# Optimization experiments

Measured on AMD Instinct MI355X. Metric: run time of the kernel, lower is better.

The kernel has to match this reference:

```python
import jax, jax.numpy as jnp
import numpy as np

# dims matching init_kwargs
D_MODEL = 2048
D_STATE = 64
D_CONV = 4
EXPAND = 2
HEADDIM = 128
NGROUPS = 1
CHUNK = 256
D_INNER = EXPAND * D_MODEL          # 4096
NHEADS = D_INNER // HEADDIM          # 32
CONV_DIM = D_INNER + 2 * NGROUPS * D_STATE      # 4224
D_IN_PROJ = 2 * D_INNER + 2 * NGROUPS * D_STATE + NHEADS  # 8352
BATCH = 2
SEQ = 4096  # multiple of CHUNK -> pad_to_block_length is a no-op
LN_EPS = 1e-5


def setup_inputs() -> dict:
    key = jax.random.key(0)
    ks = jax.random.split(key, 8)
    u = jax.random.normal(ks[0], (BATCH, SEQ, D_MODEL), jnp.float32)
    in_proj_w = jax.random.normal(ks[1], (D_IN_PROJ, D_MODEL), jnp.float32) * 0.02
    in_proj_b = jnp.zeros((D_IN_PROJ,), jnp.float32)
    conv_w = jax.random.normal(ks[2], (CONV_DIM, 1, D_CONV), jnp.float32) * 0.2
    conv_b = jnp.zeros((CONV_DIM,), jnp.float32)
    # dt_bias init as in the module (inverse-softplus of dt in [dt_min, dt_max])
    dt = jnp.exp(jax.random.uniform(ks[3], (NHEADS,), jnp.float32)
                 * (np.log(0.1) - np.log(0.001)) + np.log(0.001))
    dt_bias = dt + jnp.log(-jnp.expm1(-dt))
    A_log = jnp.log(jax.random.uniform(ks[4], (NHEADS,), jnp.float32, 1.0, 16.0))
    ln_w = jnp.ones((D_INNER,), jnp.float32)
    ln_b = jnp.zeros((D_INNER,), jnp.float32)
    out_proj_w = jax.random.normal(ks[5], (D_MODEL, D_INNER), jnp.float32) * 0.02
    out_proj_b = jnp.zeros((D_MODEL,), jnp.float32)
    return dict(u=u, in_proj_w=in_proj_w, in_proj_b=in_proj_b, conv_w=conv_w,
                conv_b=conv_b, dt_bias=dt_bias, A_log=A_log, ln_w=ln_w,
                ln_b=ln_b, out_proj_w=out_proj_w, out_proj_b=out_proj_b)


def segsum(x):
    """x: (..., T) -> (..., T, T) with segsum[i,j] = sum_{j<k<=i} x[k], -inf above diag."""
    T = x.shape[-1]
    lo = jnp.tril(jnp.ones((T, T), bool), -1)
    seg = jnp.cumsum(jnp.where(lo, x[..., :, None], 0.0), axis=-2)
    return jnp.where(jnp.tril(jnp.ones((T, T), bool), 0), seg, -jnp.inf)


def ssd_chunked(X, A, B, C):
    """X:(b,l,h,p) A:(b,l,h) B:(b,l,n) C:(b,l,n) (ngroups=1), chunked SSD scan."""
    b, l, h, p = X.shape
    c = l // CHUNK
    Xc = X.reshape(b, c, CHUNK, h, p)
    Ac = A.reshape(b, c, CHUNK, h).transpose(0, 3, 1, 2)  # b h c l
    Bc = B.reshape(b, c, CHUNK, -1)
    Cc = C.reshape(b, c, CHUNK, -1)
    A_cumsum = jnp.cumsum(Ac, axis=-1)                    # b h c l
    L = jnp.exp(segsum(Ac))                               # b h c l l
    Y_diag = jnp.einsum('bcln,bcsn,bhcls,bcshp->bclhp', Cc, Bc, L, Xc)
    decay_states = jnp.exp(A_cumsum[..., -1:] - A_cumsum)  # b h c l
    states = jnp.einsum('bcln,bhcl,bclhp->bchpn', Bc, decay_states, Xc)
    states = jnp.concatenate([jnp.zeros_like(states[:, :1]), states], axis=1)  # b (c+1) h p n
    A_last = jnp.pad(A_cumsum[..., -1], ((0, 0), (0, 0), (1, 0)))  # b h (c+1)
    decay_chunk = jnp.exp(segsum(A_last))                 # b h (c+1) (c+1)
    new_states = jnp.einsum('bhzc,bchpn->bzhpn', decay_chunk, states)
    inter_states = new_states[:, :-1]                     # b c h p n
    state_decay_out = jnp.exp(A_cumsum)                   # b h c l
    Y_off = jnp.einsum('bcln,bchpn,bhcl->bclhp', Cc, inter_states, state_decay_out)
    return (Y_diag + Y_off).reshape(b, l, h, p)


def reference(u, in_proj_w, in_proj_b, conv_w, conv_b, dt_bias, A_log,
              ln_w, ln_b, out_proj_w, out_proj_b):
    # seqlen already a multiple of CHUNK, so padding is a no-op
    zxbcdt = jnp.einsum('bld,ed->ble', u, in_proj_w) + in_proj_b
    A = -jnp.exp(A_log)                                   # (h,)
    z = zxbcdt[..., :D_INNER]
    xBC = zxbcdt[..., D_INNER:D_INNER + CONV_DIM]
    dt = jax.nn.softplus(zxbcdt[..., D_INNER + CONV_DIM:] + dt_bias)  # (b,l,h)
    # causal depthwise conv1d (pad left d_conv-1, crop to seqlen)
    x_ncl = jnp.transpose(xBC, (0, 2, 1))
    y_ncl = jax.lax.conv_general_dilated(
        x_ncl, conv_w, window_strides=(1,), padding=[(D_CONV - 1, 0)],
        feature_group_count=CONV_DIM, dimension_numbers=('NCH', 'OIH', 'NCH'))
    xBC = jax.nn.silu(jnp.transpose(y_ncl + conv_b[None, :, None], (0, 2, 1)))
    x = xBC[..., :D_INNER].reshape(*xBC.shape[:2], NHEADS, HEADDIM)  # b l h p
    Bm = xBC[..., D_INNER:D_INNER + NGROUPS * D_STATE]                # b l n
    Cm = xBC[..., D_INNER + NGROUPS * D_STATE:]                       # b l n
    y = ssd_chunked(x * dt[..., None], A * dt, Bm, Cm)
    y = y.reshape(*y.shape[:2], D_INNER)
    y = y * jax.nn.silu(z)
    mu = jnp.mean(y, axis=-1, keepdims=True)
    var = jnp.mean(jnp.square(y - mu), axis=-1, keepdims=True)
    y = (y - mu) * jax.lax.rsqrt(var + LN_EPS) * ln_w + ln_b
    out = jnp.einsum('bld,ed->ble', y, out_proj_w) + out_proj_b
    return out
```

## Files before the change

kernel.cpp:

```cpp
#include <hip/hip_runtime.h>
#include <math.h>

#define BATCH    2
#define SEQ      4096
#define DMODEL   2048
#define DSTATE   64
#define HEADDIM  128
#define NHEADS   32
#define DINNER   4096
#define CONVDIM  4224
#define DINPROJ  8352
#define NCHUNK   16
#define CHUNKL   256
#define ROWS     (BATCH*SEQ)

typedef __attribute__((ext_vector_type(8))) __bf16 bf16x8;
typedef __attribute__((ext_vector_type(4))) float floatx4;
typedef __attribute__((ext_vector_type(8))) unsigned short ushort8;
typedef __attribute__((ext_vector_type(2))) unsigned int uint2v;

__device__ __forceinline__ unsigned short f2bf(float f) {
    union { float f; unsigned int u; } v; v.f = f;
    unsigned int u = v.u;
    unsigned int r = (u + 0x7FFFu + ((u >> 16) & 1u)) >> 16;
    return (unsigned short)r;
}
__device__ __forceinline__ float bf2f(unsigned short s) {
    union { unsigned int u; float f; } v; v.u = ((unsigned int)s) << 16;
    return v.f;
}

__device__ __forceinline__ void gload_lds16(const unsigned short* g, unsigned short* lds) {
    __builtin_amdgcn_global_load_lds(
        (const __attribute__((address_space(1))) unsigned int*)g,
        (__attribute__((address_space(3))) unsigned int*)lds,
        16, 0, 0);
}

__device__ __forceinline__ uint2v tr16(const unsigned short* p) {
    uint2v d;
    asm volatile("ds_read_b64_tr_b16 %0, %1"
                 : "=v"(d)
                 : "v"((const __attribute__((address_space(3))) unsigned short*)p));
    return d;
}
union U8tr { uint2v v2[2]; bf16x8 f; };

__device__ __forceinline__ void cvt8(const float* s, unsigned short* d, int i) {
    float4 a = *reinterpret_cast<const float4*>(s + i);
    float4 b = *reinterpret_cast<const float4*>(s + i + 4);
    ushort8 o;
    o[0] = f2bf(a.x); o[1] = f2bf(a.y); o[2] = f2bf(a.z); o[3] = f2bf(a.w);
    o[4] = f2bf(b.x); o[5] = f2bf(b.y); o[6] = f2bf(b.z); o[7] = f2bf(b.w);
    *reinterpret_cast<ushort8*>(d + i) = o;
}

__global__ __launch_bounds__(256) void f32_to_bf16_2(
    const float* __restrict__ s0, unsigned short* __restrict__ d0, int nb0,
    const float* __restrict__ s1, unsigned short* __restrict__ d1)
{
    int b = blockIdx.x;
    if (b < nb0) {
        cvt8(s0, d0, (b * 256 + threadIdx.x) * 8);
    } else {
        cvt8(s1, d1, ((b - nb0) * 256 + threadIdx.x) * 8);
    }
}


#define STAGE(G, ldg, grow0, clampmax, k0, off)                                 \
  { int r0_ = (grow0) + sr0; int r1_ = (grow0) + sr1;                           \
    if ((clampmax) >= 0) { if (r0_ > (clampmax)) r0_ = (clampmax);              \
                           if (r1_ > (clampmax)) r1_ = (clampmax); }            \
    unsigned short* d_ = smem + (off) + ldsw;                                   \
    gload_lds16((G) + (size_t)r0_ * (ldg) + (k0) + sc0, d_);                    \
    gload_lds16((G) + (size_t)r1_ * (ldg) + (k0) + sc1, d_ + 4096); }

__device__ __forceinline__ void rd_a(bf16x8 (&dst)[4][2], const unsigned short* base) {
    #pragma unroll
    for (int mt = 0; mt < 4; ++mt)
        #pragma unroll
        for (int ks = 0; ks < 2; ++ks)
            dst[mt][ks] = *reinterpret_cast<const bf16x8*>(base + (mt * 2 + ks) * 512);
}
__device__ __forceinline__ void rd_b(bf16x8 (&dst)[2][2], const unsigned short* base) {
    #pragma unroll
    for (int nt = 0; nt < 2; ++nt)
        #pragma unroll
        for (int ks = 0; ks < 2; ++ks)
            dst[nt][ks] = *reinterpret_cast<const bf16x8*>(base + (nt * 2 + ks) * 512);
}

template<int R0, int C0>
__device__ __forceinline__ void mfma_q(floatx4 (&acc)[8][4],
                                       const bf16x8 (&a)[4][2],
                                       const bf16x8 (&b)[2][2])
{
    #pragma unroll
    for (int mt = 0; mt < 4; ++mt)
        #pragma unroll
        for (int nt = 0; nt < 2; ++nt) {
            acc[R0+mt][C0+nt] = __builtin_amdgcn_mfma_f32_16x16x32_bf16(a[mt][0], b[nt][0], acc[R0+mt][C0+nt], 0, 0, 0);
            acc[R0+mt][C0+nt] = __builtin_amdgcn_mfma_f32_16x16x32_bf16(a[mt][1], b[nt][1], acc[R0+mt][C0+nt], 0, 0, 0);
        }
}

template<int OUT_BF16>
__global__ __launch_bounds__(512, 2) void gemm256(
    const unsigned short* __restrict__ A, int lda,
    const unsigned short* __restrict__ Bt, int ldb,
    const float* __restrict__ bias,
    void* __restrict__ Cp, int ldc,
    int M, int N, int K)
{
    extern __shared__ __align__(16) unsigned short smem[];
    const int tid  = threadIdx.x;
    const int wave = tid >> 6;
    const int lane = tid & 63;
    const int q    = lane >> 4;
    const int lm   = lane & 15;
    const int wm   = wave >> 2;
    const int wn   = wave & 3;
    const int bh   = wn >> 1;
    const int bn2  = wn & 1;

    const int cpx = gridDim.x >> 3;
    const int sid = (blockIdx.x & 7) * cpx + (blockIdx.x >> 3);
    const int nbm = M >> 8;
    const int bm  = sid % nbm;
    const int bn  = sid / nbm;
    const int arow0 = bm * 256;
    const int brow0 = bn * 256;

    int sr0, sc0, sr1, sc1;
    {
        int L = tid << 4;
        int b = L & 1023; b ^= ((b >> 9) & 1) << 5;
        int sub = L >> 10;
        sr0 = ((sub >> 1) << 4) | (b >> 6);
        sc0 = ((sub & 1) << 5) | ((b & 63) >> 1);
        L = 8192 | (tid << 4);
        b = L & 1023; b ^= ((b >> 9) & 1) << 5;
        sub = L >> 10;
        sr1 = ((sub >> 1) << 4) | (b >> 6);
        sc1 = ((sub & 1) << 5) | ((b & 63) >> 1);
    }
    const int ldsw = wave * 512;
    const int lhw = ((((lm << 6) | (q << 4)) ^ ((lm & 8) << 2)) >> 1);
    const int NT  = K >> 6;
    const int NM1 = N - 1;

    STAGE(A,  lda, arow0,       -1,  0,  0);
    STAGE(A,  lda, arow0 + 128, -1,  0,  8192);
    STAGE(Bt, ldb, brow0,       NM1, 0,  16384);
    STAGE(Bt, ldb, brow0 + 128, NM1, 0,  24576);
    STAGE(Bt, ldb, brow0,       NM1, 64, 32768 + 16384);
    STAGE(Bt, ldb, brow0 + 128, NM1, 64, 32768 + 24576);
    STAGE(A,  lda, arow0,       -1,  64, 32768);
    STAGE(A,  lda, arow0 + 128, -1,  64, 32768 + 8192);
    asm volatile("s_waitcnt vmcnt(8)" ::: "memory");
    __builtin_amdgcn_s_barrier();

    const unsigned short* Ab0 = smem + wm * 8192 + lhw;
    const unsigned short* Bb0 = smem + 16384 + bh * 8192 + bn2 * 4096 + lhw;
    const unsigned short* Ab1 = Ab0 + 32768;
    const unsigned short* Bb1 = Bb0 + 32768;

    bf16x8 a_lo[4][2], a_hi[4][2], b_lo[2][2], b_hi[2][2];
    rd_a(a_lo, Ab0);
    rd_b(b_lo, Bb0);

    floatx4 acc[8][4] = {};
    const int NI = NT >> 1;

    for (int i = 0; i < NI; ++i) {
        int tE2 = 2 * i + 2; if (tE2 > NT - 1) tE2 = NT - 1;
        int tO2 = 2 * i + 3; if (tO2 > NT - 1) tO2 = NT - 1;
        const int kE = tE2 << 6, kO = tO2 << 6;

        rd_b(b_hi, Bb0 + 2048);
        __builtin_amdgcn_s_barrier();
        __builtin_amdgcn_s_setprio(1);
        mfma_q<0,0>(acc, a_lo, b_lo);
        __builtin_amdgcn_s_setprio(0);
        __builtin_amdgcn_s_barrier();

        rd_a(a_hi, Ab0 + 4096);
        __builtin_amdgcn_s_barrier();
        __builtin_amdgcn_s_setprio(1);
        mfma_q<0,2>(acc, a_lo, b_hi);
        __builtin_amdgcn_s_setprio(0);
        __builtin_amdgcn_s_barrier();

        STAGE(Bt, ldb, brow0,       NM1, kE, 16384);
        STAGE(Bt, ldb, brow0 + 128, NM1, kE, 24576);
        __builtin_amdgcn_s_barrier();
        __builtin_amdgcn_s_setprio(1);
        mfma_q<4,2>(acc, a_hi, b_hi);
        __builtin_amdgcn_s_setprio(0);
        asm volatile("s_waitcnt vmcnt(4)" ::: "memory");
        __builtin_amdgcn_s_barrier();

        rd_a(a_lo, Ab1);
        rd_b(b_hi, Bb1);
        STAGE(A, lda, arow0,       -1, kE, 0);
        STAGE(A, lda, arow0 + 128, -1, kE, 8192);
        __builtin_amdgcn_s_barrier();
        __builtin_amdgcn_s_setprio(1);
        mfma_q<4,0>(acc, a_hi, b_lo);
        __builtin_amdgcn_s_setprio(0);
        __builtin_amdgcn_s_barrier();

        rd_b(b_lo, Bb1 + 2048);
        __builtin_amdgcn_s_barrier();
        __builtin_amdgcn_s_setprio(1);
        mfma_q<0,0>(acc, a_lo, b_hi);
        __builtin_amdgcn_s_setprio(0);
        __builtin_amdgcn_s_barrier();

        rd_a(a_hi, Ab1 + 4096);
        __builtin_amdgcn_s_barrier();
        __builtin_amdgcn_s_setprio(1);
        mfma_q<0,2>(acc, a_lo, b_lo);
        __builtin_amdgcn_s_setprio(0);
        __builtin_amdgcn_s_barrier();

        STAGE(Bt, ldb, brow0,       NM1, kO, 32768 + 16384);
        STAGE(Bt, ldb, brow0 + 128, NM1, kO, 32768 + 24576);
        __builtin_amdgcn_s_barrier();
        __builtin_amdgcn_s_setprio(1);
        mfma_q<4,2>(acc, a_hi, b_lo);
        __builtin_amdgcn_s_setprio(0);
        asm volatile("s_waitcnt vmcnt(4)" ::: "memory");
        __builtin_amdgcn_s_barrier();

        rd_a(a_lo, Ab0);
        rd_b(b_lo, Bb0);
        STAGE(A, lda, arow0,       -1, kO, 32768);
        STAGE(A, lda, arow0 + 128, -1, kO, 32768 + 8192);
        __builtin_amdgcn_s_barrier();
        __builtin_amdgcn_s_setprio(1);
        mfma_q<4,0>(acc, a_hi, b_hi);
        __builtin_amdgcn_s_setprio(0);
        __builtin_amdgcn_s_barrier();
    }

    asm volatile("s_waitcnt vmcnt(0)" ::: "memory");

    const int row0 = arow0 + wm * 128;
    const int col0 = brow0 + wn * 64;
    #pragma unroll
    for (int mt = 0; mt < 8; ++mt)
        #pragma unroll
        for (int nt = 0; nt < 4; ++nt) {
            int col = col0 + nt * 16 + lm;
            if (col < N) {
                float bv = bias[col];
                #pragma unroll
                for (int r = 0; r < 4; ++r) {
                    int row = row0 + mt * 16 + q * 4 + r;
                    float v = acc[mt][nt][r] + bv;
                    if (OUT_BF16)
                        ((unsigned short*)Cp)[(size_t)row * ldc + col] = f2bf(v);
                    else
                        ((float*)Cp)[(size_t)row * ldc + col] = v;
                }
            }
        }
}

#define NCONVB (ROWS * (CONVDIM / 8) / 256)

__global__ __launch_bounds__(256) void convdt(
    const unsigned short* __restrict__ zx, const float* __restrict__ conv_w,
    const float* __restrict__ conv_b, unsigned short* __restrict__ xBC,
    const float* __restrict__ dt_bias, const float* __restrict__ A_log,
    float* __restrict__ dtb, float* __restrict__ cum, float* __restrict__ csum)
{
    __shared__ float ws4[4];
    if (blockIdx.x < NCONVB) {
        int idx = blockIdx.x * 256 + threadIdx.x;
        int g   = idx % (CONVDIM / 8);
        int row = idx / (CONVDIM / 8);
        int l   = row & (SEQ - 1);
        int ch0 = g * 8;
        const unsigned short* base = zx + (size_t)row * DINPROJ + DINNER + ch0;
        float s[8];
        float4 w4[8];
        #pragma unroll
        for (int c = 0; c < 8; ++c) {
            s[c]  = conv_b[ch0 + c];
            w4[c] = *reinterpret_cast<const float4*>(conv_w + (ch0 + c) * 4);
        }
        #pragma unroll
        for (int j = 0; j < 4; ++j) {
            int lj = l - 3 + j;
            if (lj >= 0) {
                ushort8 v = *reinterpret_cast<const ushort8*>(base + (long)(lj - l) * DINPROJ);
                #pragma unroll
                for (int c = 0; c < 8; ++c) {
                    float wj = (j == 0) ? w4[c].x : (j == 1) ? w4[c].y : (j == 2) ? w4[c].z : w4[c].w;
                    s[c] += wj * bf2f(v[c]);
                }
            }
        }
        ushort8 o;
        #pragma unroll
        for (int c = 0; c < 8; ++c) {
            float sig = 1.f / (1.f + __expf(-s[c]));
            o[c] = f2bf(s[c] * sig);
        }
        *reinterpret_cast<ushort8*>(xBC + (size_t)row * CONVDIM + ch0) = o;
    } else {
        int id = blockIdx.x - NCONVB;
        int h  = id & 31;
        int c  = (id >> 5) & 15;
        int b  = id >> 9;
        int t  = threadIdx.x;
        int row = b * SEQ + c * CHUNKL + t;
        float v = bf2f(zx[(size_t)row * DINPROJ + DINNER + CONVDIM + h]) + dt_bias[h];
        float dtv = (v > 20.f) ? v : log1pf(__expf(v));
        dtb[row * NHEADS + h] = dtv;
        float adt = -__expf(A_log[h]) * dtv;
        int lane = t & 63, wv = t >> 6;
        float s = adt;
        #pragma unroll
        for (int o = 1; o < 64; o <<= 1) {
            float x = __shfl_up(s, o, 64);
            if (lane >= o) s += x;
        }
        if (lane == 63) ws4[wv] = s;
        __syncthreads();
        float basev = 0.f;
        #pragma unroll
        for (int w = 0; w < 3; ++w)
            if (w < wv) basev += ws4[w];
        s += basev;
        cum[id * 256 + t] = s;
        if (t == 255) csum[id] = s;
    }
}

__global__ __launch_bounds__(256) void score_kernel(
    const unsigned short* __restrict__ xBC, unsigned short* __restrict__ S_raw)
{
    int bc = blockIdx.x;
    int sq = blockIdx.y;
    int tid = threadIdx.x;
    int wave = tid >> 6, lane = tid & 63, q = lane >> 4, lm = lane & 15;
    __shared__ __align__(16) unsigned short Ct[256 * 72];
    __shared__ __align__(16) unsigned short Btl[64 * 72];

    #pragma unroll
    for (int i = 0; i < 8; ++i) {
        int idx = tid + 256 * i;
        int r = idx >> 3, ch = idx & 7;
        ushort8 v = *reinterpret_cast<const ushort8*>(
            &xBC[(size_t)(bc * 256 + r) * CONVDIM + DINNER + DSTATE + ch * 8]);
        *reinterpret_cast<ushort8*>(&Ct[r * 72 + ch * 8]) = v;
    }
    #pragma unroll
    for (int i = 0; i < 2; ++i) {
        int idx = tid + 256 * i;
        int r = idx >> 3, ch = idx & 7;
        ushort8 v = *reinterpret_cast<const ushort8*>(
            &xBC[(size_t)(bc * 256 + sq * 64 + r) * CONVDIM + DINNER + ch * 8]);
        *reinterpret_cast<ushort8*>(&Btl[r * 72 + ch * 8]) = v;
    }
    __syncthreads();

    floatx4 acc[4][4] = {};
    #pragma unroll
    for (int ks = 0; ks < 2; ++ks) {
        bf16x8 af[4], bfv[4];
        #pragma unroll
        for (int mt = 0; mt < 4; ++mt)
            af[mt] = *reinterpret_cast<const bf16x8*>(&Ct[(wave * 64 + mt * 16 + lm) * 72 + ks * 32 + q * 8]);
        #pragma unroll
        for (int nt = 0; nt < 4; ++nt)
            bfv[nt] = *reinterpret_cast<const bf16x8*>(&Btl[(nt * 16 + lm) * 72 + ks * 32 + q * 8]);
        #pragma unroll
        for (int mt = 0; mt < 4; ++mt)
            #pragma unroll
            for (int nt = 0; nt < 4; ++nt)
                acc[mt][nt] = __builtin_amdgcn_mfma_f32_16x16x32_bf16(af[mt], bfv[nt], acc[mt][nt], 0, 0, 0);
    }

    #pragma unroll
    for (int mt = 0; mt < 4; ++mt)
        #pragma unroll
        for (int nt = 0; nt < 4; ++nt) {
            int l = wave * 64 + mt * 16 + q * 4;
            int s = sq * 64 + nt * 16 + lm;
            #pragma unroll
            for (int r = 0; r < 4; ++r)
                S_raw[(size_t)(bc * 256 + l + r) * 256 + s] = f2bf(acc[mt][nt][r]);
        }
}

__global__ __launch_bounds__(256) void states_kernel(
    const unsigned short* __restrict__ xBC, const float* __restrict__ dtb,
    const float* __restrict__ cum, float* __restrict__ states)
{
    int id = blockIdx.x;
    int h  = id & 31;
    int c  = (id >> 5) & 15;
    int b  = id >> 9;
    int tid = threadIdx.x;
    int wave = tid >> 6, lane = tid & 63, q = lane >> 4, lm = lane & 15;

    __shared__ float wls[256];
    __shared__ __align__(16) unsigned short Xs[16 * 8 * 72];
    __shared__ __align__(16) unsigned short Bs[16 * 4 * 72];

    const int cumbase = id * 256;
    const int row0 = b * SEQ + c * CHUNKL;
    {
        float cumlast = cum[cumbase + 255];
        wls[tid] = __expf(cumlast - cum[cumbase + tid]) * dtb[(row0 + tid) * NHEADS + h];
    }

    floatx4 acc[2][4] = {};

    for (int sc = 0; sc < 4; ++sc) {
        const int s0 = sc * 64;
        __syncthreads();
        #pragma unroll
        for (int i = 0; i < 4; ++i) {
            int idx = tid + 256 * i;
            int sr = idx >> 4, ch = idx & 15;
            int row = row0 + s0 + sr;
            ushort8 v = *reinterpret_cast<const ushort8*>(
                &xBC[(size_t)row * CONVDIM + h * HEADDIM + ch * 8]);
            float w = wls[s0 + sr];
            ushort8 o;
            #pragma unroll
            for (int j = 0; j < 8; ++j) o[j] = f2bf(bf2f(v[j]) * w);
            int a = ((sr >> 2) * 8 + (ch >> 1)) * 72 + (sr & 3) * 16 + (ch & 1) * 8;
            *reinterpret_cast<ushort8*>(&Xs[a]) = o;
        }
        #pragma unroll
        for (int i = 0; i < 2; ++i) {
            int idx = tid + 256 * i;
            int sr = idx >> 3, ch = idx & 7;
            int row = row0 + s0 + sr;
            ushort8 v = *reinterpret_cast<const ushort8*>(
                &xBC[(size_t)row * CONVDIM + DINNER + ch * 8]);
            int a = ((sr >> 2) * 4 + (ch >> 1)) * 72 + (sr & 3) * 16 + (ch & 1) * 8;
            *reinterpret_cast<ushort8*>(&Bs[a]) = v;
        }
        __syncthreads();
        #pragma unroll
        for (int ks = 0; ks < 2; ++ks) {
            bf16x8 af[2], bfv[4];
            #pragma unroll
            for (int mt = 0; mt < 2; ++mt) {
                const unsigned short* vp = Xs + ((ks * 8 + 2 * q) * 8 + (wave * 2 + mt)) * 72 + lm * 4;
                U8tr u; u.v2[0] = tr16(vp); u.v2[1] = tr16(vp + 576);
                af[mt] = u.f;
            }
            #pragma unroll
            for (int nt = 0; nt < 4; ++nt) {
                const unsigned short* vp = Bs + ((ks * 8 + 2 * q) * 4 + nt) * 72 + lm * 4;
                U8tr u; u.v2[0] = tr16(vp); u.v2[1] = tr16(vp + 288);
                bfv[nt] = u.f;
            }
            asm volatile("s_waitcnt lgkmcnt(0)" ::: "memory");
            __builtin_amdgcn_sched_barrier(0);
            #pragma unroll
            for (int mt = 0; mt < 2; ++mt)
                #pragma unroll
                for (int nt = 0; nt < 4; ++nt)
                    acc[mt][nt] = __builtin_amdgcn_mfma_f32_16x16x32_bf16(af[mt], bfv[nt], acc[mt][nt], 0, 0, 0);
        }
    }

    #pragma unroll
    for (int mt = 0; mt < 2; ++mt)
        #pragma unroll
        for (int nt = 0; nt < 4; ++nt)
            #pragma unroll
            for (int r = 0; r < 4; ++r) {
                int p = wave * 32 + mt * 16 + q * 4 + r;
                int n = nt * 16 + lm;
                states[(size_t)id * 8192 + p * 64 + n] = acc[mt][nt][r];
            }
}

__global__ __launch_bounds__(256) void inter_kernel(
    float* __restrict__ states, const float* __restrict__ csum)
{
    int idx = blockIdx.x * 256 + threadIdx.x;
    int pn  = idx & 8191;
    int h   = (idx >> 13) & 31;
    int b   = idx >> 18;
    float S = 0.f;
    for (int c = 0; c < 16; ++c) {
        int id = (b * 16 + c) * 32 + h;
        size_t off = (size_t)id * 8192 + pn;
        float st = states[off];
        states[off] = S;
        S = S * __expf(csum[id]) + st;
    }
}

__global__ __launch_bounds__(256) void y_mfma(
    const unsigned short* __restrict__ xBC,
    const unsigned short* __restrict__ S_raw,
    const float* __restrict__ dtb,
    const float* __restrict__ cum,
    const float* __restrict__ inter,
    unsigned short* __restrict__ zx)
{
    int id = blockIdx.x;
    int h  = id & 31;
    int bc = id >> 5;
    const int lh = blockIdx.y;
    int tid = threadIdx.x, wave = tid >> 6, lane = tid & 63, q = lane >> 4, lm = lane & 15;
    int wl = wave >> 1, wp = wave & 1;

    __shared__ float cums[256];
    __shared__ float dts[256];
    __shared__ __align__(16) unsigned short XdtT[128 * 72];
    __shared__ __align__(16) unsigned short PT[128 * 72];

    cums[tid] = cum[id * 256 + tid];
    dts[tid]  = dtb[(size_t)(bc * 256 + tid) * NHEADS + h];
    __syncthreads();

    floatx4 acc[4][4] = {};
    const int l0w = lh * 128 + wl * 64;
    const int nst = 2 * lh + 2;

    for (int st = 0; st < nst; ++st) {
        const int s0 = st * 64;
        __syncthreads();
        #pragma unroll
        for (int i = 0; i < 4; ++i) {
            int idx = tid + 256 * i;
            int sr = idx >> 4, ch = idx & 15;
            int srow = bc * 256 + s0 + sr;
            ushort8 v = *reinterpret_cast<const ushort8*>(
                &xBC[(size_t)srow * CONVDIM + h * HEADDIM + ch * 8]);
            float dt = dts[s0 + sr];
            ushort8 o;
            #pragma unroll
            for (int j = 0; j < 8; ++j) o[j] = f2bf(bf2f(v[j]) * dt);
            int a = ((sr >> 2) * 8 + (ch >> 1)) * 72 + (sr & 3) * 16 + (ch & 1) * 8;
            *reinterpret_cast<ushort8*>(&XdtT[a]) = o;
        }
        const int r0 = (s0 > lh * 128) ? 64 : 0;
        const int iters = (128 - r0) >> 5;
        for (int i = 0; i < iters; ++i) {
            int idx = tid + 256 * i;
            int r = r0 + (idx >> 3), ch = idx & 7;
            int l = lh * 128 + r;
            float cl = cums[l];
            ushort8 v = *reinterpret_cast<const ushort8*>(
                &S_raw[(size_t)(bc * 256 + l) * 256 + s0 + ch * 8]);
            ushort8 o;
            #pragma unroll
            for (int j = 0; j < 8; ++j) {
                int s = s0 + ch * 8 + j;
                float val = (s <= l) ? bf2f(v[j]) * __expf(cl - cums[s]) : 0.f;
                o[j] = f2bf(val);
            }
            *reinterpret_cast<ushort8*>(&PT[r * 72 + ch * 8]) = o;
        }
        __syncthreads();
        if (s0 <= l0w) {
            #pragma unroll
            for (int ks = 0; ks < 2; ++ks) {
                bf16x8 af[4], bfv[4];
                #pragma unroll
                for (int mt = 0; mt < 4; ++mt)
                    af[mt] = *reinterpret_cast<const bf16x8*>(
                        &PT[(wl * 64 + mt * 16 + lm) * 72 + ks * 32 + q * 8]);
                #pragma unroll
                for (int nt = 0; nt < 4; ++nt) {
                    const unsigned short* vp = XdtT + ((ks * 8 + 2 * q) * 8 + (wp * 4 + nt)) * 72 + lm * 4;
                    U8tr u; u.v2[0] = tr16(vp); u.v2[1] = tr16(vp + 576);
                    bfv[nt] = u.f;
                }
                asm volatile("s_waitcnt lgkmcnt(0)" ::: "memory");
                __builtin_amdgcn_sched_barrier(0);
                #pragma unroll
                for (int mt = 0; mt < 4; ++mt)
                    #pragma unroll
                    for (int nt = 0; nt < 4; ++nt)
                        acc[mt][nt] = __builtin_amdgcn_mfma_f32_16x16x32_bf16(af[mt], bfv[nt], acc[mt][nt], 0, 0, 0);
            }
        }
    }

    __syncthreads();
    {
        int p = tid >> 1, n0 = (tid & 1) * 32;
        const float* sp = &inter[(size_t)id * 8192 + p * 64 + n0];
        #pragma unroll
        for (int k2 = 0; k2 < 4; ++k2) {
            float4 a = *reinterpret_cast<const float4*>(sp + k2 * 8);
            float4 b2 = *reinterpret_cast<const float4*>(sp + k2 * 8 + 4);
            ushort8 o;
            o[0] = f2bf(a.x); o[1] = f2bf(a.y); o[2] = f2bf(a.z); o[3] = f2bf(a.w);
            o[4] = f2bf(b2.x); o[5] = f2bf(b2.y); o[6] = f2bf(b2.z); o[7] = f2bf(b2.w);
            *reinterpret_cast<ushort8*>(&XdtT[p * 72 + n0 + k2 * 8]) = o;
        }
        int r = tid >> 1;
        int l = lh * 128 + r;
        float ef = __expf(cums[l]);
        const unsigned short* cp = &xBC[(size_t)(bc * 256 + l) * CONVDIM + DINNER + DSTATE + n0];
        #pragma unroll
        for (int k2 = 0; k2 < 4; ++k2) {
            ushort8 v = *reinterpret_cast<const ushort8*>(cp + k2 * 8);
            ushort8 o;
            #pragma unroll
            for (int j = 0; j < 8; ++j) o[j] = f2bf(bf2f(v[j]) * ef);
            *reinterpret_cast<ushort8*>(&PT[r * 72 + n0 + k2 * 8]) = o;
        }
    }
    __syncthreads();
    #pragma unroll
    for (int ks = 0; ks < 2; ++ks) {
        bf16x8 af[4], bfv[4];
        #pragma unroll
        for (int mt = 0; mt < 4; ++mt)
            af[mt] = *reinterpret_cast<const bf16x8*>(
                &PT[(wl * 64 + mt * 16 + lm) * 72 + ks * 32 + q * 8]);
        #pragma unroll
        for (int nt = 0; nt < 4; ++nt)
            bfv[nt] = *reinterpret_cast<const bf16x8*>(
                &XdtT[(wp * 64 + nt * 16 + lm) * 72 + ks * 32 + q * 8]);
        #pragma unroll
        for (int mt = 0; mt < 4; ++mt)
            #pragma unroll
            for (int nt = 0; nt < 4; ++nt)
                acc[mt][nt] = __builtin_amdgcn_mfma_f32_16x16x32_bf16(af[mt], bfv[nt], acc[mt][nt], 0, 0, 0);
    }

    #pragma unroll
    for (int mt = 0; mt < 4; ++mt)
        #pragma unroll
        for (int nt = 0; nt < 4; ++nt) {
            int l = lh * 128 + wl * 64 + mt * 16 + q * 4;
            int pcol = wp * 64 + nt * 16 + lm;
            #pragma unroll
            for (int r = 0; r < 4; ++r)
                zx[(size_t)(bc * 256 + l + r) * DINPROJ + DINNER + h * HEADDIM + pcol]
                    = f2bf(acc[mt][nt][r]);
        }
}

__global__ __launch_bounds__(256) void gate_ln_cvt(
    unsigned short* __restrict__ zx, const float* __restrict__ ln_w,
    const float* __restrict__ ln_b,
    const float* __restrict__ w2, unsigned short* __restrict__ w2_bf)
{
    __shared__ float rs[256], rq[256];
    if (blockIdx.x >= ROWS) {
        cvt8(w2, w2_bf, ((blockIdx.x - ROWS) * 256 + threadIdx.x) * 8);
        return;
    }
    int row = blockIdx.x;
    int t   = threadIdx.x;
    size_t base = (size_t)row * DINPROJ;
    float g[16];
    float sum = 0.f, sumsq = 0.f;
    #pragma unroll
    for (int j = 0; j < 2; ++j) {
        int i = t * 8 + j * 2048;
        ushort8 zv = *reinterpret_cast<const ushort8*>(zx + base + i);
        ushort8 yv = *reinterpret_cast<const ushort8*>(zx + base + DINNER + i);
        #pragma unroll
        for (int k = 0; k < 8; ++k) {
            float z = bf2f(zv[k]);
            float y = bf2f(yv[k]);
            float sig = 1.f / (1.f + __expf(-z));
            float v = y * z * sig;
            g[j * 8 + k] = v;
            sum += v; sumsq += v * v;
        }
    }
    rs[t] = sum; rq[t] = sumsq;
    __syncthreads();
    for (int off = 128; off > 0; off >>= 1) {
        if (t < off) { rs[t] += rs[t + off]; rq[t] += rq[t + off]; }
        __syncthreads();
    }
    float mu   = rs[0] * (1.f / DINNER);
    float var  = rq[0] * (1.f / DINNER) - mu * mu;
    float rstd = rsqrtf(var + 1e-5f);
    #pragma unroll
    for (int j = 0; j < 2; ++j) {
        int i = t * 8 + j * 2048;
        ushort8 o;
        #pragma unroll
        for (int k = 0; k < 8; ++k)
            o[k] = f2bf((g[j * 8 + k] - mu) * rstd * ln_w[i + k] + ln_b[i + k]);
        *reinterpret_cast<ushort8*>(zx + base + DINNER + i) = o;
    }
}

extern "C" void kernel_launch(void* const* d_in, const int* in_sizes, int n_in,
                              void* d_out, int out_size, void* d_ws, size_t ws_size,
                              hipStream_t stream)
{
    const float* u          = (const float*)d_in[0];
    const float* in_proj_w  = (const float*)d_in[1];
    const float* in_proj_b  = (const float*)d_in[2];
    const float* conv_w     = (const float*)d_in[3];
    const float* conv_b     = (const float*)d_in[4];
    const float* dt_bias    = (const float*)d_in[5];
    const float* A_log      = (const float*)d_in[6];
    const float* ln_w       = (const float*)d_in[7];
    const float* ln_b       = (const float*)d_in[8];
    const float* out_proj_w = (const float*)d_in[9];
    const float* out_proj_b = (const float*)d_in[10];
    float* out = (float*)d_out;

    unsigned short* zx  = (unsigned short*)d_ws;
    unsigned short* xBC = zx + (size_t)ROWS * DINPROJ;
    float* dtb    = (float*)(xBC + (size_t)ROWS * CONVDIM);
    float* cum    = dtb + (size_t)ROWS * NHEADS;
    float* csum   = cum + (size_t)ROWS * NHEADS;
    float* states = csum + 1024;
    unsigned short* S_raw = (unsigned short*)(states + (size_t)1024 * 8192);

    unsigned short* u_bf  = (unsigned short*)states;
    unsigned short* w1_bf = xBC;
    unsigned short* w2_bf = (unsigned short*)states;

    static bool attr_done = false;
    if (!attr_done) {
        hipFuncSetAttribute(reinterpret_cast<const void*>(&gemm256<1>),
                            hipFuncAttributeMaxDynamicSharedMemorySize, 131072);
        hipFuncSetAttribute(reinterpret_cast<const void*>(&gemm256<0>),
                            hipFuncAttributeMaxDynamicSharedMemorySize, 131072);
        attr_done = true;
    }

    dim3 blk(256);

    const int NBU  = (ROWS * DMODEL) / 2048;
    const int NBW1 = (DINPROJ * DMODEL) / 2048;
    f32_to_bf16_2<<<dim3(NBU + NBW1), blk, 0, stream>>>(u, u_bf, NBU, in_proj_w, w1_bf);

    gemm256<1><<<dim3((ROWS / 256) * ((DINPROJ + 255) / 256)), dim3(512), 131072, stream>>>(
        u_bf, DMODEL, w1_bf, DMODEL, in_proj_b, (void*)zx, DINPROJ, ROWS, DINPROJ, DMODEL);

    convdt<<<dim3(NCONVB + BATCH * NCHUNK * NHEADS), blk, 0, stream>>>(
        zx, conv_w, conv_b, xBC, dt_bias, A_log, dtb, cum, csum);

    score_kernel<<<dim3(BATCH * NCHUNK, 4), blk, 0, stream>>>(xBC, S_raw);

    states_kernel<<<dim3(BATCH * NCHUNK * NHEADS), blk, 0, stream>>>(xBC, dtb, cum, states);

    inter_kernel<<<dim3((BATCH * NHEADS * 8192) / 256), blk, 0, stream>>>(states, csum);

    y_mfma<<<dim3(BATCH * NCHUNK * NHEADS, 2), blk, 0, stream>>>(xBC, S_raw, dtb, cum, states, zx);

    gate_ln_cvt<<<dim3(ROWS + (DMODEL * DINNER) / 2048), blk, 0, stream>>>(
        zx, ln_w, ln_b, out_proj_w, w2_bf);

    gemm256<0><<<dim3((ROWS / 256) * (DMODEL / 256)), dim3(512), 131072, stream>>>(
        (const unsigned short*)(zx + DINNER), DINPROJ, w2_bf, DINNER, out_proj_b, (void*)out,
        DMODEL, ROWS, DMODEL, DINNER);
}
```

Measured before the change: 898.0 us.

## Regroup GEMM tile swizzle, spread global stages, skip MFMA for out-of-range waves

Replaces the simple block-to-tile mapping with a grouped (GM=8) row-major swizzle to improve L2 reuse of A/B tiles. Redistributes the four STAGE global loads more evenly across the MFMA phases and adjusts the vmcnt wait. Adds an 'alive' flag so waves whose column tile lies entirely beyond N skip their MFMA work in the ragged last N tile. The grouping assumes gridDim divisible by nbm, and the changed wait count must still match the outstanding loads.

```diff
diff --git a/kernel.cpp b/kernel.cpp
--- a/kernel.cpp
+++ b/kernel.cpp
@@ -105,6 +105,11 @@
         }
 }
 
+#define MQ(R0, C0, A_, B_)                          \
+    __builtin_amdgcn_s_setprio(1);                  \
+    if (alive) mfma_q<R0, C0>(acc, A_, B_);         \
+    __builtin_amdgcn_s_setprio(0);
+
 template<int OUT_BF16>
 __global__ __launch_bounds__(512, 2) void gemm256(
     const unsigned short* __restrict__ A, int lda,
@@ -127,10 +132,20 @@
     const int cpx = gridDim.x >> 3;
     const int sid = (blockIdx.x & 7) * cpx + (blockIdx.x >> 3);
     const int nbm = M >> 8;
-    const int bm  = sid % nbm;
-    const int bn  = sid / nbm;
+    const int nbn = gridDim.x / nbm;
+    int bm, bn;
+    {
+        const int GM = 8;
+        int nig = GM * nbn;
+        int grp = sid / nig;
+        int first = grp * GM;
+        int gsz = nbm - first; if (gsz > GM) gsz = GM;
+        bm = first + (sid % nig) % gsz;
+        bn = (sid % nig) / gsz;
+    }
     const int arow0 = bm * 256;
     const int brow0 = bn * 256;
+    const bool alive = (brow0 + wn * 64) < N;
 
     int sr0, sc0, sr1, sc1;
     {
@@ -180,68 +195,52 @@
 
         rd_b(b_hi, Bb0 + 2048);
         __builtin_amdgcn_s_barrier();
-        __builtin_amdgcn_s_setprio(1);
-        mfma_q<0,0>(acc, a_lo, b_lo);
-        __builtin_amdgcn_s_setprio(0);
+        MQ(0, 0, a_lo, b_lo);
         __builtin_amdgcn_s_barrier();
 
         rd_a(a_hi, Ab0 + 4096);
-        __builtin_amdgcn_s_barrier();
-        __builtin_amdgcn_s_setprio(1);
-        mfma_q<0,2>(acc, a_lo, b_hi);
-        __builtin_amdgcn_s_setprio(0);
-        __builtin_amdgcn_s_barrier();
-
-        STAGE(Bt, ldb, brow0,       NM1, kE, 16384);
+        STAGE(Bt, ldb, brow0, NM1, kE, 16384);
+        __builtin_amdgcn_s_barrier();
+        MQ(0, 2, a_lo, b_hi);
+        __builtin_amdgcn_s_barrier();
+
         STAGE(Bt, ldb, brow0 + 128, NM1, kE, 24576);
-        __builtin_amdgcn_s_barrier();
-        __builtin_amdgcn_s_setprio(1);
-        mfma_q<4,2>(acc, a_hi, b_hi);
-        __builtin_amdgcn_s_setprio(0);
-        asm volatile("s_waitcnt vmcnt(4)" ::: "memory");
+        STAGE(A,  lda, arow0,       -1,  kE, 0);
+        __builtin_amdgcn_s_barrier();
+        MQ(4, 2, a_hi, b_hi);
+        asm volatile("s_waitcnt vmcnt(6)" ::: "memory");
         __builtin_amdgcn_s_barrier();
 
         rd_a(a_lo, Ab1);
         rd_b(b_hi, Bb1);
-        STAGE(A, lda, arow0,       -1, kE, 0);
         STAGE(A, lda, arow0 + 128, -1, kE, 8192);
         __builtin_amdgcn_s_barrier();
-        __builtin_amdgcn_s_setprio(1);
-        mfma_q<4,0>(acc, a_hi, b_lo);
-        __builtin_amdgcn_s_setprio(0);
+        MQ(4, 0, a_hi, b_lo);
         __builtin_amdgcn_s_barrier();
 
         rd_b(b_lo, Bb1 + 2048);
         __builtin_amdgcn_s_barrier();
-        __builtin_amdgcn_s_setprio(1);
-        mfma_q<0,0>(acc, a_lo, b_hi);
-        __builtin_amdgcn_s_setprio(0);
+        MQ(0, 0, a_lo, b_hi);
         __builtin_amdgcn_s_barrier();
 
         rd_a(a_hi, Ab1 + 4096);
-        __builtin_amdgcn_s_barrier();
-        __builtin_amdgcn_s_setprio(1);
-        mfma_q<0,2>(acc, a_lo, b_lo);
-        __builtin_amdgcn_s_setprio(0);
-        __builtin_amdgcn_s_barrier();
-
-        STAGE(Bt, ldb, brow0,       NM1, kO, 32768 + 16384);
+        STAGE(Bt, ldb, brow0, NM1, kO, 32768 + 16384);
+        __builtin_amdgcn_s_barrier();
+        MQ(0, 2, a_lo, b_lo);
+        __builtin_amdgcn_s_barrier();
+
         STAGE(Bt, ldb, brow0 + 128, NM1, kO, 32768 + 24576);
-        __builtin_amdgcn_s_barrier();
-        __builtin_amdgcn_s_setprio(1);
-        mfma_q<4,2>(acc, a_hi, b_lo);
-        __builtin_amdgcn_s_setprio(0);
-        asm volatile("s_waitcnt vmcnt(4)" ::: "memory");
+        STAGE(A,  lda, arow0,       -1,  kO, 32768);
+        __builtin_amdgcn_s_barrier();
+        MQ(4, 2, a_hi, b_lo);
+        asm volatile("s_waitcnt vmcnt(6)" ::: "memory");
         __builtin_amdgcn_s_barrier();
 
         rd_a(a_lo, Ab0);
         rd_b(b_lo, Bb0);
-        STAGE(A, lda, arow0,       -1, kO, 32768);
         STAGE(A, lda, arow0 + 128, -1, kO, 32768 + 8192);
         __builtin_amdgcn_s_barrier();
-        __builtin_amdgcn_s_setprio(1);
-        mfma_q<4,0>(acc, a_hi, b_hi);
-        __builtin_amdgcn_s_setprio(0);
+        MQ(4, 0, a_hi, b_hi);
         __builtin_amdgcn_s_barrier();
     }
 
```

New measurement: 889.1 us. About the same (-1.0%).
